# Optimization experiments

Measured on AMD Instinct MI355X. Metric: run time of the kernel, lower is better.

## Reference

```python
import jax, jax.numpy as jnp
import numpy as np

NUM_EXPERTS = 64
TOP_K = 8
TEMPERATURE = 1.0


def setup_inputs() -> dict:
    key = jax.random.key(0)
    k1, k2 = jax.random.split(key)
    B, D, E = 32768, 2048, NUM_EXPERTS
    r = jax.random.normal(k1, (B, D), dtype=jnp.float32)
    W = jax.random.normal(k2, (E, D), dtype=jnp.float32) * (1.0 / np.sqrt(D))
    b = jnp.zeros((E,), dtype=jnp.float32)
    return {"r": r, "W": W, "b": b}


def reference(r, W, b):
    # logits: (B, E) = r @ W^T + b, then temperature scaling
    logits = (jnp.einsum('bd,ed->be', r, W) + b) / TEMPERATURE
    weights_soft = jax.nn.softmax(logits, axis=-1)
    if TOP_K is not None and TOP_K < NUM_EXPERTS:
        topk_vals, topk_idx = jax.lax.top_k(weights_soft, TOP_K)
        mask = jnp.zeros_like(weights_soft)
        mask = jax.vmap(lambda m, i: m.at[i].set(1.0))(mask, topk_idx)
        weights_hard = weights_soft * mask
        weights_hard = weights_hard / (weights_hard.sum(axis=-1, keepdims=True) + 1e-9)
    else:
        weights_hard = weights_soft
    return (weights_hard, weights_soft)
```

## Files before the change

kernel.cpp:

```cpp
#include <hip/hip_runtime.h>
#include <hip/hip_bf16.h>
#include <stdint.h>


#define D_DIM 2048
#define E_DIM 64
#define B_DIM 32768
#define TOPK 8
#define NK 16

typedef __bf16 bf16x8 __attribute__((ext_vector_type(8)));
typedef float f32x4 __attribute__((ext_vector_type(4)));

__global__ __launch_bounds__(256) void w_prep(const float* __restrict__ W,
                                              __bf16* __restrict__ P) {
    const int K = blockIdx.x;
    const int u = threadIdx.x;
    const float* src = W + (size_t)(u >> 2) * D_DIM + K * 32 + (u & 3) * 8;
    __bf16* dst = P + (size_t)K * 6144 + u * 8;
    bf16x8 o1, o2, o3;
    #pragma unroll
    for (int j = 0; j < 8; ++j) {
        float x  = src[j];
        __bf16 h1 = (__bf16)x;
        float r1 = x - (float)h1;
        __bf16 h2 = (__bf16)r1;
        float r2 = r1 - (float)h2;
        o1[j] = h1; o2[j] = h2; o3[j] = (__bf16)r2;
    }
    *(bf16x8*)(dst)        = o1;
    *(bf16x8*)(dst + 2048) = o2;
    *(bf16x8*)(dst + 4096) = o3;
}

__global__ __launch_bounds__(256, 2) void moe_gate(const float* __restrict__ r,
                                                   const __bf16* __restrict__ P,
                                                   const float* __restrict__ bias,
                                                   float* __restrict__ out) {
    __shared__ float lg[4][16][E_DIM + 1];

    const int t    = threadIdx.x;
    const int wv   = t >> 6;
    const int lane = t & 63;
    const int lrow = lane & 15;
    const int quad = lane >> 4;
    const int row0 = blockIdx.x * 16;

    const __bf16* Pq = P + (size_t)wv * NK * 6144 + quad * 8 + lrow * 32;
    const float* ra = r + (size_t)(row0 + lrow) * D_DIM + wv * 512 + quad * 8;

    f32x4 accM[4] = {};
    f32x4 accD[4] = {};
    f32x4 accL[4] = {};

    bf16x8 B0[3][4], B1[3][4];
    float4 p00, p01, p10, p11;

#define LOADB(Bd, kk) do {                                                  \
        const __bf16* bb_ = Pq + (size_t)(kk) * 6144;                       \
        _Pragma("unroll")                                                   \
        for (int s_ = 0; s_ < 3; ++s_)                                      \
            _Pragma("unroll")                                               \
            for (int n_ = 0; n_ < 4; ++n_)                                  \
                Bd[s_][n_] = *(const bf16x8*)(bb_ + s_ * 2048 + n_ * 512);  \
    } while (0)

#define LOADA(pa_, pb_, kk) do {                                            \
        pa_ = *(const float4*)(ra + (kk) * 32);                             \
        pb_ = *(const float4*)(ra + (kk) * 32 + 4);                         \
    } while (0)

#define COMPUTE(Bd, pa_, pb_) do {                                          \
        float av_[8] = {pa_.x, pa_.y, pa_.z, pa_.w,                         \
                        pb_.x, pb_.y, pb_.z, pb_.w};                        \
        bf16x8 A1_, A2_, A3_;                                               \
        _Pragma("unroll")                                                   \
        for (int j_ = 0; j_ < 8; ++j_) {                                    \
            float x_  = av_[j_];                                            \
            __bf16 h1_ = (__bf16)x_;                                        \
            float r1_ = x_ - (float)h1_;                                    \
            __bf16 h2_ = (__bf16)r1_;                                       \
            float r2_ = r1_ - (float)h2_;                                   \
            A1_[j_] = h1_; A2_[j_] = h2_; A3_[j_] = (__bf16)r2_;            \
        }                                                                   \
        _Pragma("unroll")                                                   \
        for (int n_ = 0; n_ < 4; ++n_) {                                    \
            accM[n_] = __builtin_amdgcn_mfma_f32_16x16x32_bf16(A1_, Bd[0][n_], accM[n_], 0, 0, 0); \
            accD[n_] = __builtin_amdgcn_mfma_f32_16x16x32_bf16(A1_, Bd[1][n_], accD[n_], 0, 0, 0); \
            accD[n_] = __builtin_amdgcn_mfma_f32_16x16x32_bf16(A2_, Bd[0][n_], accD[n_], 0, 0, 0); \
            accL[n_] = __builtin_amdgcn_mfma_f32_16x16x32_bf16(A1_, Bd[2][n_], accL[n_], 0, 0, 0); \
            accL[n_] = __builtin_amdgcn_mfma_f32_16x16x32_bf16(A2_, Bd[1][n_], accL[n_], 0, 0, 0); \
            accL[n_] = __builtin_amdgcn_mfma_f32_16x16x32_bf16(A3_, Bd[0][n_], accL[n_], 0, 0, 0); \
        }                                                                   \
    } while (0)

    LOADB(B0, 0); LOADA(p00, p01, 0);
    LOADB(B1, 1); LOADA(p10, p11, 1);

    #pragma unroll
    for (int ks = 0; ks < NK; ks += 2) {
        const int k2 = (ks + 2 < NK) ? ks + 2 : ks;
        const int k3 = (ks + 3 < NK) ? ks + 3 : ks + 1;

        COMPUTE(B0, p00, p01);
        LOADB(B0, k2); LOADA(p00, p01, k2);

        COMPUTE(B1, p10, p11);
        LOADB(B1, k3); LOADA(p10, p11, k3);
    }

#undef LOADB
#undef LOADA
#undef COMPUTE

    #pragma unroll
    for (int n = 0; n < 4; ++n) {
        int col = n * 16 + lrow;
        #pragma unroll
        for (int i = 0; i < 4; ++i)
            lg[wv][quad * 4 + i][col] = accM[n][i] + (accD[n][i] + accL[n][i]);
    }
    __syncthreads();

    const float bcol = bias[lane];
    for (int rr = wv; rr < 16; rr += 4) {
        float logit = ((lg[0][rr][lane] + lg[1][rr][lane]) +
                       (lg[2][rr][lane] + lg[3][rr][lane])) + bcol;
        float mx = logit;
        #pragma unroll
        for (int s = 32; s >= 1; s >>= 1) mx = fmaxf(mx, __shfl_xor(mx, s));
        float ex = expf(logit - mx);
        float sm = ex;
        #pragma unroll
        for (int s = 32; s >= 1; s >>= 1) sm += __shfl_xor(sm, s);
        float soft = ex / sm;

        bool  sel    = false;
        float topsum = 0.0f;
        #pragma unroll
        for (int it = 0; it < TOPK; ++it) {
            float cand = sel ? -1.0f : soft;
            float cm = cand;
            #pragma unroll
            for (int s = 32; s >= 1; s >>= 1) cm = fmaxf(cm, __shfl_xor(cm, s));
            unsigned long long ball = __ballot(cand == cm);
            int leader = __ffsll(ball) - 1;
            if (lane == leader) sel = true;
            topsum += cm;
        }
        float hard = sel ? soft / (topsum + 1e-9f) : 0.0f;

        size_t orow = (size_t)(row0 + rr) * E_DIM + lane;
        out[orow] = hard;
        out[(size_t)B_DIM * E_DIM + orow] = soft;
    }
}

extern "C" void kernel_launch(void* const* d_in, const int* in_sizes, int n_in,
                              void* d_out, int out_size, void* d_ws, size_t ws_size,
                              hipStream_t stream) {
    const float* r = (const float*)d_in[0];
    const float* W = (const float*)d_in[1];
    const float* b = (const float*)d_in[2];
    float* out = (float*)d_out;
    __bf16* P = (__bf16*)d_ws;

    w_prep<<<64, 256, 0, stream>>>(W, P);
    moe_gate<<<2048, 256, 0, stream>>>(r, P, b, out);
}
```

Measured before the change: 457.5 us.

## Process 32 rows per block to reuse B fragments across two row tiles

Each block now handles two 16-row tiles, so every loaded W fragment feeds two sets of MFMAs and the W reload traffic per row is halved. The D and L correction accumulators are merged into one, and the loop drops full unrolling in favour of an explicit peeled tail with sched_barrier fences to control instruction scheduling. The grid halves to 1024 blocks. In exchange, register pressure rises from the extra accumulators and doubled A buffers, which may hurt occupancy under launch_bounds(256,2), and the merged accumulator changes summation order slightly.

```diff
diff --git a/kernel.cpp b/kernel.cpp
--- a/kernel.cpp
+++ b/kernel.cpp
@@ -37,24 +37,24 @@
                                                    const __bf16* __restrict__ P,
                                                    const float* __restrict__ bias,
                                                    float* __restrict__ out) {
-    __shared__ float lg[4][16][E_DIM + 1];
+    __shared__ float lg[4][32][E_DIM + 4];
 
     const int t    = threadIdx.x;
     const int wv   = t >> 6;
     const int lane = t & 63;
     const int lrow = lane & 15;
     const int quad = lane >> 4;
-    const int row0 = blockIdx.x * 16;
+    const int row0 = blockIdx.x * 32;
 
     const __bf16* Pq = P + (size_t)wv * NK * 6144 + quad * 8 + lrow * 32;
-    const float* ra = r + (size_t)(row0 + lrow) * D_DIM + wv * 512 + quad * 8;
+    const float* ra0 = r + (size_t)(row0 + lrow) * D_DIM + wv * 512 + quad * 8;
+    const float* ra1 = ra0 + (size_t)16 * D_DIM;
 
-    f32x4 accM[4] = {};
-    f32x4 accD[4] = {};
-    f32x4 accL[4] = {};
+    f32x4 accM[2][4]  = {};
+    f32x4 accDL[2][4] = {};
 
     bf16x8 B0[3][4], B1[3][4];
-    float4 p00, p01, p10, p11;
+    float4 A0[2][2], A1[2][2];
 
 #define LOADB(Bd, kk) do {                                                  \
         const __bf16* bb_ = Pq + (size_t)(kk) * 6144;                       \
@@ -65,65 +65,82 @@
                 Bd[s_][n_] = *(const bf16x8*)(bb_ + s_ * 2048 + n_ * 512);  \
     } while (0)
 
-#define LOADA(pa_, pb_, kk) do {                                            \
-        pa_ = *(const float4*)(ra + (kk) * 32);                             \
-        pb_ = *(const float4*)(ra + (kk) * 32 + 4);                         \
+#define LOADA(Ad, kk) do {                                                  \
+        Ad[0][0] = *(const float4*)(ra0 + (kk) * 32);                       \
+        Ad[0][1] = *(const float4*)(ra0 + (kk) * 32 + 4);                   \
+        Ad[1][0] = *(const float4*)(ra1 + (kk) * 32);                       \
+        Ad[1][1] = *(const float4*)(ra1 + (kk) * 32 + 4);                   \
     } while (0)
 
-#define COMPUTE(Bd, pa_, pb_) do {                                          \
-        float av_[8] = {pa_.x, pa_.y, pa_.z, pa_.w,                         \
-                        pb_.x, pb_.y, pb_.z, pb_.w};                        \
-        bf16x8 A1_, A2_, A3_;                                               \
+#define COMPUTE(Bd, Ad) do {                                                \
         _Pragma("unroll")                                                   \
-        for (int j_ = 0; j_ < 8; ++j_) {                                    \
-            float x_  = av_[j_];                                            \
-            __bf16 h1_ = (__bf16)x_;                                        \
-            float r1_ = x_ - (float)h1_;                                    \
-            __bf16 h2_ = (__bf16)r1_;                                       \
-            float r2_ = r1_ - (float)h2_;                                   \
-            A1_[j_] = h1_; A2_[j_] = h2_; A3_[j_] = (__bf16)r2_;            \
-        }                                                                   \
-        _Pragma("unroll")                                                   \
-        for (int n_ = 0; n_ < 4; ++n_) {                                    \
-            accM[n_] = __builtin_amdgcn_mfma_f32_16x16x32_bf16(A1_, Bd[0][n_], accM[n_], 0, 0, 0); \
-            accD[n_] = __builtin_amdgcn_mfma_f32_16x16x32_bf16(A1_, Bd[1][n_], accD[n_], 0, 0, 0); \
-            accD[n_] = __builtin_amdgcn_mfma_f32_16x16x32_bf16(A2_, Bd[0][n_], accD[n_], 0, 0, 0); \
-            accL[n_] = __builtin_amdgcn_mfma_f32_16x16x32_bf16(A1_, Bd[2][n_], accL[n_], 0, 0, 0); \
-            accL[n_] = __builtin_amdgcn_mfma_f32_16x16x32_bf16(A2_, Bd[1][n_], accL[n_], 0, 0, 0); \
-            accL[n_] = __builtin_amdgcn_mfma_f32_16x16x32_bf16(A3_, Bd[0][n_], accL[n_], 0, 0, 0); \
+        for (int rt_ = 0; rt_ < 2; ++rt_) {                                 \
+            float av_[8] = {Ad[rt_][0].x, Ad[rt_][0].y, Ad[rt_][0].z,       \
+                            Ad[rt_][0].w, Ad[rt_][1].x, Ad[rt_][1].y,       \
+                            Ad[rt_][1].z, Ad[rt_][1].w};                    \
+            bf16x8 A1_, A2_, A3_;                                           \
+            _Pragma("unroll")                                               \
+            for (int j_ = 0; j_ < 8; ++j_) {                                \
+                float x_  = av_[j_];                                        \
+                __bf16 h1_ = (__bf16)x_;                                    \
+                float r1_ = x_ - (float)h1_;                                \
+                __bf16 h2_ = (__bf16)r1_;                                   \
+                float r2_ = r1_ - (float)h2_;                               \
+                A1_[j_] = h1_; A2_[j_] = h2_; A3_[j_] = (__bf16)r2_;        \
+            }                                                               \
+            _Pragma("unroll")                                               \
+            for (int n_ = 0; n_ < 4; ++n_)                                  \
+                accM[rt_][n_]  = __builtin_amdgcn_mfma_f32_16x16x32_bf16(A1_, Bd[0][n_], accM[rt_][n_], 0, 0, 0);  \
+            _Pragma("unroll")                                               \
+            for (int n_ = 0; n_ < 4; ++n_)                                  \
+                accDL[rt_][n_] = __builtin_amdgcn_mfma_f32_16x16x32_bf16(A1_, Bd[1][n_], accDL[rt_][n_], 0, 0, 0); \
+            _Pragma("unroll")                                               \
+            for (int n_ = 0; n_ < 4; ++n_)                                  \
+                accDL[rt_][n_] = __builtin_amdgcn_mfma_f32_16x16x32_bf16(A2_, Bd[0][n_], accDL[rt_][n_], 0, 0, 0); \
+            _Pragma("unroll")                                               \
+            for (int n_ = 0; n_ < 4; ++n_)                                  \
+                accDL[rt_][n_] = __builtin_amdgcn_mfma_f32_16x16x32_bf16(A1_, Bd[2][n_], accDL[rt_][n_], 0, 0, 0); \
+            _Pragma("unroll")                                               \
+            for (int n_ = 0; n_ < 4; ++n_)                                  \
+                accDL[rt_][n_] = __builtin_amdgcn_mfma_f32_16x16x32_bf16(A2_, Bd[1][n_], accDL[rt_][n_], 0, 0, 0); \
+            _Pragma("unroll")                                               \
+            for (int n_ = 0; n_ < 4; ++n_)                                  \
+                accDL[rt_][n_] = __builtin_amdgcn_mfma_f32_16x16x32_bf16(A3_, Bd[0][n_], accDL[rt_][n_], 0, 0, 0); \
         }                                                                   \
     } while (0)
 
-    LOADB(B0, 0); LOADA(p00, p01, 0);
-    LOADB(B1, 1); LOADA(p10, p11, 1);
+    LOADB(B0, 0); LOADA(A0, 0);
+    LOADB(B1, 1); LOADA(A1, 1);
+    __builtin_amdgcn_sched_barrier(0);
 
-    #pragma unroll
-    for (int ks = 0; ks < NK; ks += 2) {
-        const int k2 = (ks + 2 < NK) ? ks + 2 : ks;
-        const int k3 = (ks + 3 < NK) ? ks + 3 : ks + 1;
-
-        COMPUTE(B0, p00, p01);
-        LOADB(B0, k2); LOADA(p00, p01, k2);
-
-        COMPUTE(B1, p10, p11);
-        LOADB(B1, k3); LOADA(p10, p11, k3);
+    for (int ks = 0; ks <= NK - 4; ks += 2) {
+        COMPUTE(B0, A0);
+        LOADB(B0, ks + 2); LOADA(A0, ks + 2);
+        __builtin_amdgcn_sched_barrier(0);
+        COMPUTE(B1, A1);
+        LOADB(B1, ks + 3); LOADA(A1, ks + 3);
+        __builtin_amdgcn_sched_barrier(0);
     }
+    COMPUTE(B0, A0);
+    COMPUTE(B1, A1);
 
 #undef LOADB
 #undef LOADA
 #undef COMPUTE
 
     #pragma unroll
-    for (int n = 0; n < 4; ++n) {
-        int col = n * 16 + lrow;
+    for (int rt = 0; rt < 2; ++rt)
         #pragma unroll
-        for (int i = 0; i < 4; ++i)
-            lg[wv][quad * 4 + i][col] = accM[n][i] + (accD[n][i] + accL[n][i]);
-    }
+        for (int n = 0; n < 4; ++n) {
+            int col = n * 16 + lrow;
+            #pragma unroll
+            for (int i = 0; i < 4; ++i)
+                lg[wv][rt * 16 + quad * 4 + i][col] = accM[rt][n][i] + accDL[rt][n][i];
+        }
     __syncthreads();
 
     const float bcol = bias[lane];
-    for (int rr = wv; rr < 16; rr += 4) {
+    for (int rr = wv; rr < 32; rr += 4) {
         float logit = ((lg[0][rr][lane] + lg[1][rr][lane]) +
                        (lg[2][rr][lane] + lg[3][rr][lane])) + bcol;
         float mx = logit;
@@ -166,5 +183,5 @@
     __bf16* P = (__bf16*)d_ws;
 
     w_prep<<<64, 256, 0, stream>>>(W, P);
-    moe_gate<<<2048, 256, 0, stream>>>(r, P, b, out);
+    moe_gate<<<1024, 256, 0, stream>>>(r, P, b, out);
 }
```

Result: faster. 402.8 us (-12.0%).

## Stage W splits in LDS and give each wave its own 16 rows over full K

Applied to the files above, without the earlier changes.

Each block now handles 64 rows, and each wave owns 16 rows across the whole K range. The block previously handled 16 rows with a split-K reduction over four waves. The three-way bf16 split of W is double-buffered into LDS with global_load_lds and shared by all four waves, with waitcnt plus barrier at every K step, instead of each wave loading its own W slice from global. The D and L accumulators are merged into one to free registers, and the grid drops to 512 blocks. This cuts redundant W traffic and the cross-wave logit reduction, but adds a barrier per step and leaves fewer blocks to fill the GPU.

```diff
diff --git a/kernel.cpp b/kernel.cpp
--- a/kernel.cpp
+++ b/kernel.cpp
@@ -7,7 +7,7 @@
 #define E_DIM 64
 #define B_DIM 32768
 #define TOPK 8
-#define NK 16
+#define NKS 64
 
 typedef __bf16 bf16x8 __attribute__((ext_vector_type(8)));
 typedef float f32x4 __attribute__((ext_vector_type(4)));
@@ -33,47 +33,69 @@
     *(bf16x8*)(dst + 4096) = o3;
 }
 
+__device__ __forceinline__ void gload_lds16(const void* g, void* s) {
+    __builtin_amdgcn_global_load_lds(
+        (const __attribute__((address_space(1))) unsigned int*)g,
+        (__attribute__((address_space(3))) unsigned int*)s,
+        16, 0, 0);
+}
+
+__device__ __forceinline__ void fence_barrier() {
+    __builtin_amdgcn_sched_barrier(0);
+    __builtin_amdgcn_s_barrier();
+    __builtin_amdgcn_sched_barrier(0);
+}
+
 __global__ __launch_bounds__(256, 2) void moe_gate(const float* __restrict__ r,
                                                    const __bf16* __restrict__ P,
                                                    const float* __restrict__ bias,
                                                    float* __restrict__ out) {
-    __shared__ float lg[4][16][E_DIM + 1];
+    __shared__ __bf16 bstage[2][3][2048];
+    __shared__ float  lg[64][E_DIM + 1];
 
     const int t    = threadIdx.x;
     const int wv   = t >> 6;
     const int lane = t & 63;
     const int lrow = lane & 15;
     const int quad = lane >> 4;
-    const int row0 = blockIdx.x * 16;
+    const int row0 = blockIdx.x * 64;
 
-    const __bf16* Pq = P + (size_t)wv * NK * 6144 + quad * 8 + lrow * 32;
-    const float* ra = r + (size_t)(row0 + lrow) * D_DIM + wv * 512 + quad * 8;
+    const __bf16* Pt = P + t * 8;
+    const float* ra = r + (size_t)(row0 + wv * 16 + lrow) * D_DIM + quad * 8;
+    const int fo = quad * 8 + lrow * 32;
 
-    f32x4 accM[4] = {};
-    f32x4 accD[4] = {};
-    f32x4 accL[4] = {};
+    f32x4 accM[4]  = {};
+    f32x4 accDL[4] = {};
 
-    bf16x8 B0[3][4], B1[3][4];
-    float4 p00, p01, p10, p11;
+    float4 Aa0, Aa1, Ab0, Ab1;
 
-#define LOADB(Bd, kk) do {                                                  \
-        const __bf16* bb_ = Pq + (size_t)(kk) * 6144;                       \
+    #pragma unroll
+    for (int s = 0; s < 3; ++s)
+        gload_lds16(Pt + s * 2048, &bstage[0][s][t * 8]);
+    Aa0 = *(const float4*)(ra);
+    Aa1 = *(const float4*)(ra + 4);
+    Ab0 = *(const float4*)(ra + 32);
+    Ab1 = *(const float4*)(ra + 36);
+    asm volatile("s_waitcnt vmcnt(4)" ::: "memory");
+    fence_barrier();
+
+#define ITER(CUR, NXT, A0_, A1_, kk) do {                                   \
+        if ((kk) + 1 < NKS) {                                               \
+            _Pragma("unroll")                                               \
+            for (int s_ = 0; s_ < 3; ++s_)                                  \
+                gload_lds16(Pt + (size_t)((kk) + 1) * 6144 + s_ * 2048,     \
+                            &bstage[NXT][s_][t * 8]);                       \
+        }                                                                   \
+        bf16x8 Bf[3][4];                                                    \
         _Pragma("unroll")                                                   \
         for (int s_ = 0; s_ < 3; ++s_)                                      \
             _Pragma("unroll")                                               \
             for (int n_ = 0; n_ < 4; ++n_)                                  \
-                Bd[s_][n_] = *(const bf16x8*)(bb_ + s_ * 2048 + n_ * 512);  \
-    } while (0)
-
-#define LOADA(pa_, pb_, kk) do {                                            \
-        pa_ = *(const float4*)(ra + (kk) * 32);                             \
-        pb_ = *(const float4*)(ra + (kk) * 32 + 4);                         \
-    } while (0)
-
-#define COMPUTE(Bd, pa_, pb_) do {                                          \
-        float av_[8] = {pa_.x, pa_.y, pa_.z, pa_.w,                         \
-                        pb_.x, pb_.y, pb_.z, pb_.w};                        \
-        bf16x8 A1_, A2_, A3_;                                               \
+                Bf[s_][n_] = *(const bf16x8*)(&bstage[CUR][0][0] +          \
+                                              s_ * 2048 + n_ * 512 + fo);   \
+        float av_[8] = {A0_.x, A0_.y, A0_.z, A0_.w,                         \
+                        A1_.x, A1_.y, A1_.z, A1_.w};                        \
+        bf16x8 A1f, A2f, A3f;                                               \
         _Pragma("unroll")                                                   \
         for (int j_ = 0; j_ < 8; ++j_) {                                    \
             float x_  = av_[j_];                                            \
@@ -81,51 +103,54 @@
             float r1_ = x_ - (float)h1_;                                    \
             __bf16 h2_ = (__bf16)r1_;                                       \
             float r2_ = r1_ - (float)h2_;                                   \
-            A1_[j_] = h1_; A2_[j_] = h2_; A3_[j_] = (__bf16)r2_;            \
+            A1f[j_] = h1_; A2f[j_] = h2_; A3f[j_] = (__bf16)r2_;            \
+        }                                                                   \
+        {    \
+            const int k2_ = ((kk) + 2 < NKS) ? (kk) + 2 : (kk);             \
+            A0_ = *(const float4*)(ra + k2_ * 32);                          \
+            A1_ = *(const float4*)(ra + k2_ * 32 + 4);                      \
         }                                                                   \
         _Pragma("unroll")                                                   \
-        for (int n_ = 0; n_ < 4; ++n_) {                                    \
-            accM[n_] = __builtin_amdgcn_mfma_f32_16x16x32_bf16(A1_, Bd[0][n_], accM[n_], 0, 0, 0); \
-            accD[n_] = __builtin_amdgcn_mfma_f32_16x16x32_bf16(A1_, Bd[1][n_], accD[n_], 0, 0, 0); \
-            accD[n_] = __builtin_amdgcn_mfma_f32_16x16x32_bf16(A2_, Bd[0][n_], accD[n_], 0, 0, 0); \
-            accL[n_] = __builtin_amdgcn_mfma_f32_16x16x32_bf16(A1_, Bd[2][n_], accL[n_], 0, 0, 0); \
-            accL[n_] = __builtin_amdgcn_mfma_f32_16x16x32_bf16(A2_, Bd[1][n_], accL[n_], 0, 0, 0); \
-            accL[n_] = __builtin_amdgcn_mfma_f32_16x16x32_bf16(A3_, Bd[0][n_], accL[n_], 0, 0, 0); \
-        }                                                                   \
+        for (int n_ = 0; n_ < 4; ++n_)                                      \
+            accM[n_]  = __builtin_amdgcn_mfma_f32_16x16x32_bf16(A1f, Bf[0][n_], accM[n_], 0, 0, 0);  \
+        _Pragma("unroll")                                                   \
+        for (int n_ = 0; n_ < 4; ++n_)                                      \
+            accDL[n_] = __builtin_amdgcn_mfma_f32_16x16x32_bf16(A1f, Bf[1][n_], accDL[n_], 0, 0, 0); \
+        _Pragma("unroll")                                                   \
+        for (int n_ = 0; n_ < 4; ++n_)                                      \
+            accDL[n_] = __builtin_amdgcn_mfma_f32_16x16x32_bf16(A2f, Bf[0][n_], accDL[n_], 0, 0, 0); \
+        _Pragma("unroll")                                                   \
+        for (int n_ = 0; n_ < 4; ++n_)                                      \
+            accDL[n_] = __builtin_amdgcn_mfma_f32_16x16x32_bf16(A1f, Bf[2][n_], accDL[n_], 0, 0, 0); \
+        _Pragma("unroll")                                                   \
+        for (int n_ = 0; n_ < 4; ++n_)                                      \
+            accDL[n_] = __builtin_amdgcn_mfma_f32_16x16x32_bf16(A2f, Bf[1][n_], accDL[n_], 0, 0, 0); \
+        _Pragma("unroll")                                                   \
+        for (int n_ = 0; n_ < 4; ++n_)                                      \
+            accDL[n_] = __builtin_amdgcn_mfma_f32_16x16x32_bf16(A3f, Bf[0][n_], accDL[n_], 0, 0, 0); \
+         \
+        asm volatile("s_waitcnt vmcnt(2)" ::: "memory");                    \
+        fence_barrier();                                                    \
     } while (0)
 
-    LOADB(B0, 0); LOADA(p00, p01, 0);
-    LOADB(B1, 1); LOADA(p10, p11, 1);
-
-    #pragma unroll
-    for (int ks = 0; ks < NK; ks += 2) {
-        const int k2 = (ks + 2 < NK) ? ks + 2 : ks;
-        const int k3 = (ks + 3 < NK) ? ks + 3 : ks + 1;
-
-        COMPUTE(B0, p00, p01);
-        LOADB(B0, k2); LOADA(p00, p01, k2);
-
-        COMPUTE(B1, p10, p11);
-        LOADB(B1, k3); LOADA(p10, p11, k3);
+    for (int ks = 0; ks < NKS; ks += 2) {
+        ITER(0, 1, Aa0, Aa1, ks);
+        ITER(1, 0, Ab0, Ab1, ks + 1);
     }
-
-#undef LOADB
-#undef LOADA
-#undef COMPUTE
+#undef ITER
 
     #pragma unroll
     for (int n = 0; n < 4; ++n) {
         int col = n * 16 + lrow;
         #pragma unroll
         for (int i = 0; i < 4; ++i)
-            lg[wv][quad * 4 + i][col] = accM[n][i] + (accD[n][i] + accL[n][i]);
+            lg[wv * 16 + quad * 4 + i][col] = accM[n][i] + accDL[n][i];
     }
     __syncthreads();
 
     const float bcol = bias[lane];
-    for (int rr = wv; rr < 16; rr += 4) {
-        float logit = ((lg[0][rr][lane] + lg[1][rr][lane]) +
-                       (lg[2][rr][lane] + lg[3][rr][lane])) + bcol;
+    for (int rr = wv; rr < 64; rr += 4) {
+        float logit = lg[rr][lane] + bcol;
         float mx = logit;
         #pragma unroll
         for (int s = 32; s >= 1; s >>= 1) mx = fmaxf(mx, __shfl_xor(mx, s));
@@ -166,5 +191,5 @@
     __bf16* P = (__bf16*)d_ws;
 
     w_prep<<<64, 256, 0, stream>>>(W, P);
-    moe_gate<<<2048, 256, 0, stream>>>(r, P, b, out);
+    moe_gate<<<512, 256, 0, stream>>>(r, P, b, out);
 }
```

Result: faster. 442.6 us (-3.3%).
